# Kernel optimization log

Hardware: AMD Instinct MI355X
Metric: run time of the kernel (lower is better)

Reference implementation:

```python
import jax, jax.numpy as jnp
import numpy as np

B, T, I, H, O = 256, 100, 1024, 2048, 10

def setup_inputs() -> dict:
    key = jax.random.key(0)
    k = jax.random.split(key, 6)
    return {
        "x": jax.random.normal(k[0], (B, T, I), dtype=jnp.float32),
        "h0": jax.random.normal(k[1], (B, H), dtype=jnp.float32),
        "Win": jax.random.uniform(k[2], (I, H), dtype=jnp.float32, minval=-0.1, maxval=0.1),
        "W": jax.random.normal(k[3], (H, H), dtype=jnp.float32) * 0.01,
        "lin_w": jax.random.normal(k[4], (O, H), dtype=jnp.float32) * 0.02,
        "lin_b": jax.random.normal(k[5], (O,), dtype=jnp.float32) * 0.02,
    }

def reference(x, h0, Win, W, lin_w, lin_b):
    xin = jnp.einsum('bti,ih->bth', x, Win)  # precompute input projection for all steps

    def step(h, xin_t):
        h = jnp.tanh(xin_t + h @ W)
        y = h @ lin_w.T + lin_b
        return h, y

    _, ys = jax.lax.scan(step, h0, jnp.swapaxes(xin, 0, 1))  # ys: [T, B, O]
    return jnp.swapaxes(ys, 0, 1)  # [B, T, O]
```

## Files before the change

### kernel.cpp

```cpp
#include <hip/hip_runtime.h>
#include <math.h>

#define Bn 256
#define Tn 100
#define In 1024
#define Hn 2048
#define On 10
#define Kc (In + Hn)

typedef short s8v  __attribute__((ext_vector_type(8)));
typedef unsigned short us4 __attribute__((ext_vector_type(4)));
typedef float f32x4 __attribute__((ext_vector_type(4)));

__device__ __forceinline__ unsigned short f2bf(float f) {
    unsigned int u = __float_as_uint(f);
    u += 0x7fffu + ((u >> 16) & 1u);
    return (unsigned short)(u >> 16);
}


__global__ void conv_x_kernel(const float4* __restrict__ src, ushort4* __restrict__ dst) {
    int i = blockIdx.x * 256 + threadIdx.x;
    float4 v = src[i];
    ushort4 o;
    o.x = f2bf(v.x); o.y = f2bf(v.y); o.z = f2bf(v.z); o.w = f2bf(v.w);
    dst[i] = o;
}

__global__ void transpose_bf16_kernel(const float* __restrict__ src, unsigned short* __restrict__ dst,
                                      int N, int ld, int colOff) {
    __shared__ float tile[32][33];
    int k0 = blockIdx.x * 32;
    int n0 = blockIdx.y * 32;
    int c = threadIdx.x & 31;
    int r = threadIdx.x >> 5;
    #pragma unroll
    for (int i = 0; i < 32; i += 8)
        tile[r + i][c] = src[(size_t)(k0 + r + i) * N + n0 + c];
    __syncthreads();
    #pragma unroll
    for (int i = 0; i < 32; i += 8)
        dst[(size_t)(n0 + r + i) * ld + colOff + k0 + c] = f2bf(tile[c][r + i]);
}

__global__ void small_conv_kernel(const float* __restrict__ h0, const float* __restrict__ lin_w,
                                  unsigned short* __restrict__ h_all0, unsigned short* __restrict__ lwb,
                                  unsigned int* __restrict__ bar) {
    int idx = blockIdx.x * 256 + threadIdx.x;
    if (idx < 512) bar[idx] = 0u;
    if (idx < Bn * Hn) {
        h_all0[idx] = f2bf(h0[idx]);
    } else {
        int j = idx - Bn * Hn;
        int o = j >> 11;
        int k = j & 2047;
        lwb[j] = (o < On) ? f2bf(lin_w[o * Hn + k]) : (unsigned short)0;
    }
}

__global__ __launch_bounds__(512, 2)
void scan_kernel(const unsigned short* __restrict__ xb,
                 const unsigned short* __restrict__ BTm,
                 unsigned short* __restrict__ h_all,
                 unsigned int* __restrict__ bar) {
    const int g = blockIdx.x;
    const int m0 = ((g >> 3) & 3) * 64;
    const int n0 = ((g & 7) * 8 + (g >> 5)) * 32;
    const int w = threadIdx.x >> 6;
    const int lane = threadIdx.x & 63;
    const int quad = lane >> 4;
    const int lr = lane & 15;

    __shared__ float red[4][64][36];

    const unsigned short* bp0 = BTm + (size_t)(n0 + lr) * Kc;
    const unsigned short* bp1 = BTm + (size_t)(n0 + 16 + lr) * Kc;

    const size_t xrow = (size_t)Tn * In;

    unsigned int* grp_cnt = bar + (g & 7) * 32;
    unsigned int* mst_cnt = bar + 256;
    unsigned int* epoch   = bar + 288;

    s8v bx[4][2];
    s8v bh[8][2];
    #pragma unroll
    for (int c = 0; c < 4; ++c) {
        const int kq = w * 128 + c * 32 + quad * 8;
        bx[c][0] = *(const s8v*)(bp0 + kq);
        bx[c][1] = *(const s8v*)(bp1 + kq);
    }
    #pragma unroll
    for (int c = 0; c < 8; ++c) {
        const int kq = In + w * 256 + c * 32 + quad * 8;
        bh[c][0] = *(const s8v*)(bp0 + kq);
        bh[c][1] = *(const s8v*)(bp1 + kq);
    }

    f32x4 acc[4][2];
    #pragma unroll
    for (int mi = 0; mi < 4; ++mi)
        #pragma unroll
        for (int ni = 0; ni < 2; ++ni)
            acc[mi][ni] = (f32x4){0.f, 0.f, 0.f, 0.f};

    {
        const unsigned short* xt = xb + 0 * In;
        #pragma unroll
        for (int c = 0; c < 4; ++c) {
            const int kq = w * 128 + c * 32 + quad * 8;
            const unsigned short* arow = xt + kq + (size_t)(m0 + lr) * xrow;
            s8v a0 = *(const s8v*)(arow);
            s8v a1 = *(const s8v*)(arow + 16 * xrow);
            s8v a2 = *(const s8v*)(arow + 32 * xrow);
            s8v a3 = *(const s8v*)(arow + 48 * xrow);
            acc[0][0] = __builtin_amdgcn_mfma_f32_16x16x32_bf16(a0, bx[c][0], acc[0][0], 0, 0, 0);
            acc[1][0] = __builtin_amdgcn_mfma_f32_16x16x32_bf16(a1, bx[c][0], acc[1][0], 0, 0, 0);
            acc[2][0] = __builtin_amdgcn_mfma_f32_16x16x32_bf16(a2, bx[c][0], acc[2][0], 0, 0, 0);
            acc[3][0] = __builtin_amdgcn_mfma_f32_16x16x32_bf16(a3, bx[c][0], acc[3][0], 0, 0, 0);
            acc[0][1] = __builtin_amdgcn_mfma_f32_16x16x32_bf16(a0, bx[c][1], acc[0][1], 0, 0, 0);
            acc[1][1] = __builtin_amdgcn_mfma_f32_16x16x32_bf16(a1, bx[c][1], acc[1][1], 0, 0, 0);
            acc[2][1] = __builtin_amdgcn_mfma_f32_16x16x32_bf16(a2, bx[c][1], acc[2][1], 0, 0, 0);
            acc[3][1] = __builtin_amdgcn_mfma_f32_16x16x32_bf16(a3, bx[c][1], acc[3][1], 0, 0, 0);
        }
    }

    for (int t = 0; t < Tn; ++t) {
        const unsigned short* hprev = h_all + (size_t)t * (Bn * Hn);
        #pragma unroll
        for (int c = 0; c < 8; ++c) {
            const int kq = w * 256 + c * 32 + quad * 8;
            const unsigned short* arow = hprev + kq + (size_t)(m0 + lr) * Hn;
            s8v a0 = *(const s8v*)(arow);
            s8v a1 = *(const s8v*)(arow + 16 * Hn);
            s8v a2 = *(const s8v*)(arow + 32 * Hn);
            s8v a3 = *(const s8v*)(arow + 48 * Hn);
            acc[0][0] = __builtin_amdgcn_mfma_f32_16x16x32_bf16(a0, bh[c][0], acc[0][0], 0, 0, 0);
            acc[1][0] = __builtin_amdgcn_mfma_f32_16x16x32_bf16(a1, bh[c][0], acc[1][0], 0, 0, 0);
            acc[2][0] = __builtin_amdgcn_mfma_f32_16x16x32_bf16(a2, bh[c][0], acc[2][0], 0, 0, 0);
            acc[3][0] = __builtin_amdgcn_mfma_f32_16x16x32_bf16(a3, bh[c][0], acc[3][0], 0, 0, 0);
            acc[0][1] = __builtin_amdgcn_mfma_f32_16x16x32_bf16(a0, bh[c][1], acc[0][1], 0, 0, 0);
            acc[1][1] = __builtin_amdgcn_mfma_f32_16x16x32_bf16(a1, bh[c][1], acc[1][1], 0, 0, 0);
            acc[2][1] = __builtin_amdgcn_mfma_f32_16x16x32_bf16(a2, bh[c][1], acc[2][1], 0, 0, 0);
            acc[3][1] = __builtin_amdgcn_mfma_f32_16x16x32_bf16(a3, bh[c][1], acc[3][1], 0, 0, 0);
        }

        if (w < 4) {
            #pragma unroll
            for (int mi = 0; mi < 4; ++mi)
                #pragma unroll
                for (int ni = 0; ni < 2; ++ni)
                    #pragma unroll
                    for (int rr = 0; rr < 4; ++rr)
                        red[w][mi * 16 + quad * 4 + rr][ni * 16 + lr] = acc[mi][ni][rr];
        }
        __syncthreads();
        if (w >= 4) {
            #pragma unroll
            for (int mi = 0; mi < 4; ++mi)
                #pragma unroll
                for (int ni = 0; ni < 2; ++ni)
                    #pragma unroll
                    for (int rr = 0; rr < 4; ++rr)
                        red[w - 4][mi * 16 + quad * 4 + rr][ni * 16 + lr] += acc[mi][ni][rr];
        }
        __syncthreads();

        {
            int j = threadIdx.x << 2;
            int row = j >> 5;
            int c0 = j & 31;
            float4 s0 = *(const float4*)&red[0][row][c0];
            float4 s1 = *(const float4*)&red[1][row][c0];
            float4 s2 = *(const float4*)&red[2][row][c0];
            float4 s3 = *(const float4*)&red[3][row][c0];
            us4 o4;
            o4[0] = f2bf(tanhf(s0.x + s1.x + s2.x + s3.x));
            o4[1] = f2bf(tanhf(s0.y + s1.y + s2.y + s3.y));
            o4[2] = f2bf(tanhf(s0.z + s1.z + s2.z + s3.z));
            o4[3] = f2bf(tanhf(s0.w + s1.w + s2.w + s3.w));
            unsigned long long* dst = (unsigned long long*)
                (h_all + (size_t)(t + 1) * (Bn * Hn) + (size_t)(m0 + row) * Hn + n0 + c0);
            __hip_atomic_store(dst, __builtin_bit_cast(unsigned long long, o4),
                               __ATOMIC_RELAXED, __HIP_MEMORY_SCOPE_AGENT);
        }

        if (t < Tn - 1) {
            #pragma unroll
            for (int mi = 0; mi < 4; ++mi)
                #pragma unroll
                for (int ni = 0; ni < 2; ++ni)
                    acc[mi][ni] = (f32x4){0.f, 0.f, 0.f, 0.f};
            const unsigned short* xt = xb + (size_t)(t + 1) * In;
            #pragma unroll
            for (int c = 0; c < 4; ++c) {
                const int kq = w * 128 + c * 32 + quad * 8;
                const unsigned short* arow = xt + kq + (size_t)(m0 + lr) * xrow;
                s8v a0 = *(const s8v*)(arow);
                s8v a1 = *(const s8v*)(arow + 16 * xrow);
                s8v a2 = *(const s8v*)(arow + 32 * xrow);
                s8v a3 = *(const s8v*)(arow + 48 * xrow);
                acc[0][0] = __builtin_amdgcn_mfma_f32_16x16x32_bf16(a0, bx[c][0], acc[0][0], 0, 0, 0);
                acc[1][0] = __builtin_amdgcn_mfma_f32_16x16x32_bf16(a1, bx[c][0], acc[1][0], 0, 0, 0);
                acc[2][0] = __builtin_amdgcn_mfma_f32_16x16x32_bf16(a2, bx[c][0], acc[2][0], 0, 0, 0);
                acc[3][0] = __builtin_amdgcn_mfma_f32_16x16x32_bf16(a3, bx[c][0], acc[3][0], 0, 0, 0);
                acc[0][1] = __builtin_amdgcn_mfma_f32_16x16x32_bf16(a0, bx[c][1], acc[0][1], 0, 0, 0);
                acc[1][1] = __builtin_amdgcn_mfma_f32_16x16x32_bf16(a1, bx[c][1], acc[1][1], 0, 0, 0);
                acc[2][1] = __builtin_amdgcn_mfma_f32_16x16x32_bf16(a2, bx[c][1], acc[2][1], 0, 0, 0);
                acc[3][1] = __builtin_amdgcn_mfma_f32_16x16x32_bf16(a3, bx[c][1], acc[3][1], 0, 0, 0);
            }

            __syncthreads();
            if (threadIdx.x == 0) {
                const unsigned int tp1 = (unsigned int)(t + 1);
                unsigned int old = __hip_atomic_fetch_add(grp_cnt, 1u, __ATOMIC_RELAXED,
                                                          __HIP_MEMORY_SCOPE_AGENT);
                if (old == 32u * tp1 - 1u) {
                    unsigned int mo = __hip_atomic_fetch_add(mst_cnt, 1u, __ATOMIC_RELAXED,
                                                             __HIP_MEMORY_SCOPE_AGENT);
                    if (mo == 8u * tp1 - 1u)
                        __hip_atomic_store(epoch, tp1, __ATOMIC_RELAXED,
                                           __HIP_MEMORY_SCOPE_AGENT);
                }
                while (__hip_atomic_load(epoch, __ATOMIC_RELAXED,
                                         __HIP_MEMORY_SCOPE_AGENT) < tp1)
                    __builtin_amdgcn_s_sleep(2);
            }
            __syncthreads();
        }
    }
}

__global__ __launch_bounds__(256)
void gemm2_kernel(const unsigned short* __restrict__ h_all, const unsigned short* __restrict__ lwb,
                  const float* __restrict__ lb, float* __restrict__ y) {
    int gw = blockIdx.x * 4 + (threadIdx.x >> 6);
    int lane = threadIdx.x & 63, quad = lane >> 4, lr = lane & 15;
    int m0 = gw * 16;
    int t = m0 >> 8;
    int b0 = m0 & 255;
    const unsigned short* ah = h_all + ((size_t)(t + 1) * Bn + b0 + lr) * Hn + quad * 8;
    const unsigned short* bh = lwb + (size_t)lr * Hn + quad * 8;
    f32x4 acc0 = {0.f, 0.f, 0.f, 0.f}, acc1 = {0.f, 0.f, 0.f, 0.f};
    #pragma unroll
    for (int k0 = 0; k0 < Hn; k0 += 64) {
        s8v a0 = *(const s8v*)(ah + k0);
        s8v b0 = *(const s8v*)(bh + k0);
        acc0 = __builtin_amdgcn_mfma_f32_16x16x32_bf16(a0, b0, acc0, 0, 0, 0);
        s8v a1 = *(const s8v*)(ah + k0 + 32);
        s8v b1 = *(const s8v*)(bh + k0 + 32);
        acc1 = __builtin_amdgcn_mfma_f32_16x16x32_bf16(a1, b1, acc1, 0, 0, 0);
    }
    acc0 = acc0 + acc1;
    if (lr < On) {
        float bias = lb[lr];
        #pragma unroll
        for (int rr = 0; rr < 4; ++rr) {
            int b = b0 + quad * 4 + rr;
            y[(size_t)b * (Tn * On) + t * On + lr] = acc0[rr] + bias;
        }
    }
}


extern "C" void kernel_launch(void* const* d_in, const int* in_sizes, int n_in,
                              void* d_out, int out_size, void* d_ws, size_t ws_size,
                              hipStream_t stream) {
    const float* x   = (const float*)d_in[0];
    const float* h0  = (const float*)d_in[1];
    const float* Win = (const float*)d_in[2];
    const float* W   = (const float*)d_in[3];
    const float* lw  = (const float*)d_in[4];
    const float* lb  = (const float*)d_in[5];
    float* y = (float*)d_out;

    unsigned short* ws    = (unsigned short*)d_ws;
    unsigned short* xb    = ws;
    unsigned short* BTm   = xb + (size_t)Bn * Tn * In;
    unsigned short* h_all = BTm + (size_t)Hn * Kc;
    unsigned short* lwb   = h_all + (size_t)(Tn + 1) * Bn * Hn;
    unsigned int*   bar   = (unsigned int*)(lwb + 32768);

    conv_x_kernel<<<25600, 256, 0, stream>>>((const float4*)x, (ushort4*)xb);
    transpose_bf16_kernel<<<dim3(32, 64), 256, 0, stream>>>(Win, BTm, Hn, Kc, 0);
    transpose_bf16_kernel<<<dim3(64, 64), 256, 0, stream>>>(W, BTm, Hn, Kc, In);
    small_conv_kernel<<<2176, 256, 0, stream>>>(h0, lw, h_all, lwb, bar);

    scan_kernel<<<256, 512, 0, stream>>>(xb, BTm, h_all, bar);

    gemm2_kernel<<<400, 256, 0, stream>>>(h_all, lwb, lb, y);
}
```

Before: 1.530 ms.

## Group grid barrier by hardware XCD and use fast exp2-based tanh

Reads the hardware XCD id with s_getreg and groups the per-step grid barrier counters by the XCD each block actually runs on, counting population per XCD at startup instead of assuming a fixed block-to-XCD mapping. The aim is to keep the first-level barrier atomics local to one die's L2. Also replaces tanhf with an exp2/rcp approximation and swaps the atomic h store for a plain vector store, relying on a release fetch_add for visibility. This adds a startup all-block rendezvous and may slightly change tanh accuracy.

```diff
diff --git a/kernel.cpp b/kernel.cpp
--- a/kernel.cpp
+++ b/kernel.cpp
@@ -16,6 +16,11 @@
     unsigned int u = __float_as_uint(f);
     u += 0x7fffu + ((u >> 16) & 1u);
     return (unsigned short)(u >> 16);
+}
+
+__device__ __forceinline__ float ftanh(float x) {
+    float e = exp2f(x * 2.885390081777927f);
+    return 1.f - 2.f * __builtin_amdgcn_rcpf(e + 1.f);
 }
 
 
@@ -78,9 +83,29 @@
 
     const size_t xrow = (size_t)Tn * In;
 
-    unsigned int* grp_cnt = bar + (g & 7) * 32;
     unsigned int* mst_cnt = bar + 256;
     unsigned int* epoch   = bar + 288;
+    unsigned int* initcnt = bar + 320;
+    unsigned int* pop     = bar + 384;
+
+    unsigned int my_xcd = 0, my_pop = 0, n_xcd = 0;
+    unsigned int* grp_cnt = bar;
+    if (threadIdx.x == 0) {
+        unsigned int x_id;
+        asm volatile("s_getreg_b32 %0, hwreg(20, 0, 32)" : "=s"(x_id));
+        my_xcd = x_id & 7u;
+        grp_cnt = bar + my_xcd * 32;
+        __hip_atomic_fetch_add(pop + my_xcd, 1u, __ATOMIC_RELAXED, __HIP_MEMORY_SCOPE_AGENT);
+        __hip_atomic_fetch_add(initcnt, 1u, __ATOMIC_RELAXED, __HIP_MEMORY_SCOPE_AGENT);
+        while (__hip_atomic_load(initcnt, __ATOMIC_RELAXED, __HIP_MEMORY_SCOPE_AGENT) < 256u)
+            __builtin_amdgcn_s_sleep(2);
+        #pragma unroll
+        for (int i = 0; i < 8; ++i) {
+            unsigned int p = __hip_atomic_load(pop + i, __ATOMIC_RELAXED, __HIP_MEMORY_SCOPE_AGENT);
+            if (i == (int)my_xcd) my_pop = p;
+            if (p != 0u) ++n_xcd;
+        }
+    }
 
     s8v bx[4][2];
     s8v bh[8][2];
@@ -105,7 +130,7 @@
             acc[mi][ni] = (f32x4){0.f, 0.f, 0.f, 0.f};
 
     {
-        const unsigned short* xt = xb + 0 * In;
+        const unsigned short* xt = xb;
         #pragma unroll
         for (int c = 0; c < 4; ++c) {
             const int kq = w * 128 + c * 32 + quad * 8;
@@ -175,14 +200,11 @@
             float4 s2 = *(const float4*)&red[2][row][c0];
             float4 s3 = *(const float4*)&red[3][row][c0];
             us4 o4;
-            o4[0] = f2bf(tanhf(s0.x + s1.x + s2.x + s3.x));
-            o4[1] = f2bf(tanhf(s0.y + s1.y + s2.y + s3.y));
-            o4[2] = f2bf(tanhf(s0.z + s1.z + s2.z + s3.z));
-            o4[3] = f2bf(tanhf(s0.w + s1.w + s2.w + s3.w));
-            unsigned long long* dst = (unsigned long long*)
-                (h_all + (size_t)(t + 1) * (Bn * Hn) + (size_t)(m0 + row) * Hn + n0 + c0);
-            __hip_atomic_store(dst, __builtin_bit_cast(unsigned long long, o4),
-                               __ATOMIC_RELAXED, __HIP_MEMORY_SCOPE_AGENT);
+            o4[0] = f2bf(ftanh(s0.x + s1.x + s2.x + s3.x));
+            o4[1] = f2bf(ftanh(s0.y + s1.y + s2.y + s3.y));
+            o4[2] = f2bf(ftanh(s0.z + s1.z + s2.z + s3.z));
+            o4[3] = f2bf(ftanh(s0.w + s1.w + s2.w + s3.w));
+            *(us4*)(h_all + (size_t)(t + 1) * (Bn * Hn) + (size_t)(m0 + row) * Hn + n0 + c0) = o4;
         }
 
         if (t < Tn - 1) {
@@ -215,10 +237,10 @@
                 const unsigned int tp1 = (unsigned int)(t + 1);
                 unsigned int old = __hip_atomic_fetch_add(grp_cnt, 1u, __ATOMIC_RELAXED,
                                                           __HIP_MEMORY_SCOPE_AGENT);
-                if (old == 32u * tp1 - 1u) {
-                    unsigned int mo = __hip_atomic_fetch_add(mst_cnt, 1u, __ATOMIC_RELAXED,
+                if (old == my_pop * tp1 - 1u) {
+                    unsigned int mo = __hip_atomic_fetch_add(mst_cnt, 1u, __ATOMIC_RELEASE,
                                                              __HIP_MEMORY_SCOPE_AGENT);
-                    if (mo == 8u * tp1 - 1u)
+                    if (mo == n_xcd * tp1 - 1u)
                         __hip_atomic_store(epoch, tp1, __ATOMIC_RELAXED,
                                            __HIP_MEMORY_SCOPE_AGENT);
                 }
```

Result: slower. 1.588 ms (+3.8%).

## Replace global epoch barrier with per-row-group flag polling and use fast tanh

Applied to the files above, without the earlier changes.

Replaces the hierarchical atomic-counter grid barrier with per-block flag slots. Each block publishes its step number, and wave 0 polls the 64 slots of its own batch row group with a ballot, so blocks only wait on the producers of the rows they read rather than on the whole grid. This cuts atomic serialization and global barrier latency on every recurrence step. It also swaps tanhf for an exp2-and-reciprocal approximation, which loses some accuracy, and the relaxed-ordering correctness of the per-group wait relies on the existing store and fence semantics.

```diff
diff --git a/kernel.cpp b/kernel.cpp
--- a/kernel.cpp
+++ b/kernel.cpp
@@ -16,6 +16,11 @@
     unsigned int u = __float_as_uint(f);
     u += 0x7fffu + ((u >> 16) & 1u);
     return (unsigned short)(u >> 16);
+}
+
+__device__ __forceinline__ float ftanh(float x) {
+    float e = exp2f(x * 2.885390081777927f);
+    return 1.f - 2.f * __builtin_amdgcn_rcpf(e + 1.f);
 }
 
 
@@ -64,8 +69,10 @@
                  unsigned short* __restrict__ h_all,
                  unsigned int* __restrict__ bar) {
     const int g = blockIdx.x;
-    const int m0 = ((g >> 3) & 3) * 64;
-    const int n0 = ((g & 7) * 8 + (g >> 5)) * 32;
+    const int mgrp = (g >> 3) & 3;
+    const int m0 = mgrp * 64;
+    const int nid = (g & 7) * 8 + (g >> 5);
+    const int n0 = nid * 32;
     const int w = threadIdx.x >> 6;
     const int lane = threadIdx.x & 63;
     const int quad = lane >> 4;
@@ -78,9 +85,8 @@
 
     const size_t xrow = (size_t)Tn * In;
 
-    unsigned int* grp_cnt = bar + (g & 7) * 32;
-    unsigned int* mst_cnt = bar + 256;
-    unsigned int* epoch   = bar + 288;
+    unsigned int* myslot = bar + mgrp * 64 + nid;
+    unsigned int* grpbase = bar + mgrp * 64;
 
     s8v bx[4][2];
     s8v bh[8][2];
@@ -105,7 +111,7 @@
             acc[mi][ni] = (f32x4){0.f, 0.f, 0.f, 0.f};
 
     {
-        const unsigned short* xt = xb + 0 * In;
+        const unsigned short* xt = xb;
         #pragma unroll
         for (int c = 0; c < 4; ++c) {
             const int kq = w * 128 + c * 32 + quad * 8;
@@ -175,10 +181,10 @@
             float4 s2 = *(const float4*)&red[2][row][c0];
             float4 s3 = *(const float4*)&red[3][row][c0];
             us4 o4;
-            o4[0] = f2bf(tanhf(s0.x + s1.x + s2.x + s3.x));
-            o4[1] = f2bf(tanhf(s0.y + s1.y + s2.y + s3.y));
-            o4[2] = f2bf(tanhf(s0.z + s1.z + s2.z + s3.z));
-            o4[3] = f2bf(tanhf(s0.w + s1.w + s2.w + s3.w));
+            o4[0] = f2bf(ftanh(s0.x + s1.x + s2.x + s3.x));
+            o4[1] = f2bf(ftanh(s0.y + s1.y + s2.y + s3.y));
+            o4[2] = f2bf(ftanh(s0.z + s1.z + s2.z + s3.z));
+            o4[3] = f2bf(ftanh(s0.w + s1.w + s2.w + s3.w));
             unsigned long long* dst = (unsigned long long*)
                 (h_all + (size_t)(t + 1) * (Bn * Hn) + (size_t)(m0 + row) * Hn + n0 + c0);
             __hip_atomic_store(dst, __builtin_bit_cast(unsigned long long, o4),
@@ -211,20 +217,18 @@
             }
 
             __syncthreads();
-            if (threadIdx.x == 0) {
+            if (threadIdx.x == 0)
+                __hip_atomic_store(myslot, (unsigned int)(t + 1),
+                                   __ATOMIC_RELAXED, __HIP_MEMORY_SCOPE_AGENT);
+            if (w == 0) {
                 const unsigned int tp1 = (unsigned int)(t + 1);
-                unsigned int old = __hip_atomic_fetch_add(grp_cnt, 1u, __ATOMIC_RELAXED,
-                                                          __HIP_MEMORY_SCOPE_AGENT);
-                if (old == 32u * tp1 - 1u) {
-                    unsigned int mo = __hip_atomic_fetch_add(mst_cnt, 1u, __ATOMIC_RELAXED,
-                                                             __HIP_MEMORY_SCOPE_AGENT);
-                    if (mo == 8u * tp1 - 1u)
-                        __hip_atomic_store(epoch, tp1, __ATOMIC_RELAXED,
-                                           __HIP_MEMORY_SCOPE_AGENT);
+                unsigned int* s = grpbase + lane;
+                for (;;) {
+                    unsigned int v = __hip_atomic_load(s, __ATOMIC_RELAXED,
+                                                       __HIP_MEMORY_SCOPE_AGENT);
+                    if (__ballot(v < tp1) == 0ull) break;
+                    __builtin_amdgcn_s_sleep(1);
                 }
-                while (__hip_atomic_load(epoch, __ATOMIC_RELAXED,
-                                         __HIP_MEMORY_SCOPE_AGENT) < tp1)
-                    __builtin_amdgcn_s_sleep(2);
             }
             __syncthreads();
         }
```

Result: no change. 1.542 ms (+0.8%).
